# Performance work log

Measured on AMD Instinct MI355X. Metric: run time of the kernel, lower is better.

Reference implementation:

```python
import jax, jax.numpy as jnp
import numpy as np

D_CLAMP = 10.0
EPS = 1e-4
Z = 10.0


def setup_inputs() -> dict:
    key = jax.random.key(0)
    ks = jax.random.split(key, 7)
    b, N = 2, 512
    return {
        "predicted_rotations": jax.random.normal(ks[0], (b, N, 3, 3), dtype=jnp.float32),
        "predicted_translations": jax.random.normal(ks[1], (b, N, 3), dtype=jnp.float32),
        "predicted_atom_positions": jax.random.normal(ks[2], (b, N, 14, 3), dtype=jnp.float32),
        "atom_mask": jax.random.uniform(ks[3], (b, N, 14), dtype=jnp.float32),
        "true_rotations": jax.random.normal(ks[4], (b, N, 3, 3), dtype=jnp.float32),
        "true_translations": jax.random.normal(ks[5], (b, N, 3), dtype=jnp.float32),
        "true_atom_positions": jax.random.normal(ks[6], (b, N, 14, 3), dtype=jnp.float32),
    }


def reference(predicted_rotations, predicted_translations, predicted_atom_positions,
              atom_mask, true_rotations, true_translations, true_atom_positions):
    b, N = predicted_rotations.shape[:2]
    pred_pos = predicted_atom_positions.reshape(b, N * 14, 3)   # [b, A, 3]
    true_pos = true_atom_positions.reshape(b, N * 14, 3)
    mask = atom_mask.reshape(b, N * 14)                          # [b, A]

    # Inverse rigid transforms: R^-1 = R^T, t^-1 = -R^T t
    R_pred_inv = jnp.swapaxes(predicted_rotations, -1, -2)       # [b, N, 3, 3]
    t_pred_inv = -jnp.einsum('birc,bic->bir', R_pred_inv, predicted_translations)
    R_true_inv = jnp.swapaxes(true_rotations, -1, -2)
    t_true_inv = -jnp.einsum('birc,bic->bir', R_true_inv, true_translations)

    # Express every atom in every frame's local coordinates: [b, N, A, 3]
    x_frames_pred = jnp.einsum('biop,bjp->bijo', R_pred_inv, pred_pos) + t_pred_inv[:, :, None, :]
    x_frames_true = jnp.einsum('biop,bjp->bijo', R_true_inv, true_pos) + t_true_inv[:, :, None, :]

    dist = jnp.sqrt(jnp.sum((x_frames_pred - x_frames_true) ** 2, axis=-1) + EPS)  # [b, N, A]
    dist_clamped = jnp.minimum(dist, D_CLAMP)

    n_atoms = jnp.maximum(jnp.sum(mask, axis=-1, keepdims=True), 1.0)              # [b, 1]
    frame_means = jnp.sum(dist_clamped * mask[:, None, :], axis=-1) / n_atoms      # [b, N]
    fape_loss = jnp.mean(frame_means, axis=-1) / Z                                 # [b]
    return fape_loss
```

## Files before the change

kernel.cpp:

```cpp
#include <hip/hip_runtime.h>

#define FAPE_EPS   1e-4f
#define FAPE_CLAMP 10.0f
#define FAPE_Z     10.0f

constexpr int TPB   = 256;
constexpr int FPB   = 8;
constexpr int APT   = 8;
constexpr int ATILE = TPB * APT;
constexpr int GRPSZ = 16;
constexpr int MAXG  = 1024;

typedef float v2f __attribute__((ext_vector_type(2)));
static __device__ __forceinline__ v2f splat2(float x) { return (v2f){x, x}; }

__device__ unsigned g_gt[MAXG] = {};
__device__ unsigned g_st       = 0;

__device__ __forceinline__ v2f blockReduce2(v2f v, v2f* swave, int tid) {
    for (int off = 32; off > 0; off >>= 1) {
        v.x += __shfl_down(v.x, off);
        v.y += __shfl_down(v.y, off);
    }
    if ((tid & 63) == 0) swave[tid >> 6] = v;
    __syncthreads();
    v2f s = (v2f){0.f, 0.f};
    if (tid == 0) {
#pragma unroll
        for (int w = 0; w < TPB / 64; ++w) s += swave[w];
    }
    __syncthreads();
    return s;
}

__global__ __launch_bounds__(TPB) void fape_fused_kernel(
        const float* __restrict__ Rp, const float* __restrict__ tp,
        const float* __restrict__ pp, const float* __restrict__ mask,
        const float* __restrict__ Rt, const float* __restrict__ tt,
        const float* __restrict__ pt, float* __restrict__ out,
        float* __restrict__ ws, int N, int A,
        int fTilesPerBatch, int atomTiles, int b,
        unsigned nBlocks, unsigned nGroups) {

    const int tid   = threadIdx.x;
    const int t     = blockIdx.x;
    const int atile = t % atomTiles;
    const int ft    = t / atomTiles;
    const int batch = ft / fTilesPerBatch;
    const int ftile = ft % fTilesPerBatch;
    const int f0    = ftile * FPB;
    const int P     = fTilesPerBatch * atomTiles;

    float* __restrict__ partial  = ws;
    float* __restrict__ maskPart = ws + nBlocks;

    const float* __restrict__ ppb = pp   + (size_t)batch * A * 3;
    const float* __restrict__ ptb = pt   + (size_t)batch * A * 3;
    const float* __restrict__ mb  = mask + (size_t)batch * A;

    v2f pX[4], pY[4], pZ[4], qX[4], qY[4], qZ[4], m2[4];
    const int j0 = atile * ATILE + tid * APT;
    if (j0 + APT <= A) {
        const float4* p4 = reinterpret_cast<const float4*>(ppb + (size_t)j0 * 3);
        const float4* q4 = reinterpret_cast<const float4*>(ptb + (size_t)j0 * 3);
        const float4 P0 = p4[0], P1 = p4[1], P2 = p4[2];
        const float4 P3 = p4[3], P4 = p4[4], P5 = p4[5];
        const float4 Q0 = q4[0], Q1 = q4[1], Q2 = q4[2];
        const float4 Q3 = q4[3], Q4 = q4[4], Q5 = q4[5];
        const float4 M0 = *reinterpret_cast<const float4*>(mb + j0);
        const float4 M1 = *reinterpret_cast<const float4*>(mb + j0 + 4);
        pX[0]=(v2f){P0.x,P0.w}; pY[0]=(v2f){P0.y,P1.x}; pZ[0]=(v2f){P0.z,P1.y};
        pX[1]=(v2f){P1.z,P2.y}; pY[1]=(v2f){P1.w,P2.z}; pZ[1]=(v2f){P2.x,P2.w};
        pX[2]=(v2f){P3.x,P3.w}; pY[2]=(v2f){P3.y,P4.x}; pZ[2]=(v2f){P3.z,P4.y};
        pX[3]=(v2f){P4.z,P5.y}; pY[3]=(v2f){P4.w,P5.z}; pZ[3]=(v2f){P5.x,P5.w};
        qX[0]=(v2f){Q0.x,Q0.w}; qY[0]=(v2f){Q0.y,Q1.x}; qZ[0]=(v2f){Q0.z,Q1.y};
        qX[1]=(v2f){Q1.z,Q2.y}; qY[1]=(v2f){Q1.w,Q2.z}; qZ[1]=(v2f){Q2.x,Q2.w};
        qX[2]=(v2f){Q3.x,Q3.w}; qY[2]=(v2f){Q3.y,Q4.x}; qZ[2]=(v2f){Q3.z,Q4.y};
        qX[3]=(v2f){Q4.z,Q5.y}; qY[3]=(v2f){Q4.w,Q5.z}; qZ[3]=(v2f){Q5.x,Q5.w};
        m2[0]=(v2f){M0.x,M0.y}; m2[1]=(v2f){M0.z,M0.w};
        m2[2]=(v2f){M1.x,M1.y}; m2[3]=(v2f){M1.z,M1.w};
    } else {
        float ps[APT][3], qs[APT][3], ms[APT];
#pragma unroll
        for (int k = 0; k < APT; ++k) {
            const int j = j0 + k;
            if (j < A) {
                ps[k][0]=ppb[j*3+0]; ps[k][1]=ppb[j*3+1]; ps[k][2]=ppb[j*3+2];
                qs[k][0]=ptb[j*3+0]; qs[k][1]=ptb[j*3+1]; qs[k][2]=ptb[j*3+2];
                ms[k]=mb[j];
            } else {
                ps[k][0]=ps[k][1]=ps[k][2]=0.f;
                qs[k][0]=qs[k][1]=qs[k][2]=0.f;
                ms[k]=0.f;
            }
        }
#pragma unroll
        for (int g = 0; g < 4; ++g) {
            pX[g]=(v2f){ps[2*g][0], ps[2*g+1][0]};
            pY[g]=(v2f){ps[2*g][1], ps[2*g+1][1]};
            pZ[g]=(v2f){ps[2*g][2], ps[2*g+1][2]};
            qX[g]=(v2f){qs[2*g][0], qs[2*g+1][0]};
            qY[g]=(v2f){qs[2*g][1], qs[2*g+1][1]};
            qZ[g]=(v2f){qs[2*g][2], qs[2*g+1][2]};
            m2[g]=(v2f){ms[2*g], ms[2*g+1]};
        }
    }

    const v2f epsv   = splat2(FAPE_EPS);
    const v2f clampv = splat2(FAPE_CLAMP);
    v2f lacc = (v2f){0.f, 0.f};
    for (int f = 0; f < FPB; ++f) {
        const int fl = f0 + f;
        if (fl < N) {
            const size_t fi = (size_t)batch * N + fl;
            const float* __restrict__ rp = Rp + fi * 9;
            const float* __restrict__ rt = Rt + fi * 9;
            const float* __restrict__ tv = tp + fi * 3;
            const float* __restrict__ uv = tt + fi * 3;

            const float rp00=rp[0], rp01=rp[1], rp02=rp[2];
            const float rp10=rp[3], rp11=rp[4], rp12=rp[5];
            const float rp20=rp[6], rp21=rp[7], rp22=rp[8];
            const float rt00=rt[0], rt01=rt[1], rt02=rt[2];
            const float rt10=rt[3], rt11=rt[4], rt12=rt[5];
            const float rt20=rt[6], rt21=rt[7], rt22=rt[8];
            const float tp0=tv[0], tp1=tv[1], tp2=tv[2];
            const float tt0=uv[0], tt1=uv[1], tt2=uv[2];

            const float c0 = rt00*tt0 + rt10*tt1 + rt20*tt2 - (rp00*tp0 + rp10*tp1 + rp20*tp2);
            const float c1 = rt01*tt0 + rt11*tt1 + rt21*tt2 - (rp01*tp0 + rp11*tp1 + rp21*tp2);
            const float c2 = rt02*tt0 + rt12*tt1 + rt22*tt2 - (rp02*tp0 + rp12*tp1 + rp22*tp2);
            const v2f c0v = splat2(c0), c1v = splat2(c1), c2v = splat2(c2);

#pragma unroll
            for (int g = 0; g < 4; ++g) {
                v2f x0 = c0v + rp00*pX[g] + rp10*pY[g] + rp20*pZ[g]
                             - (rt00*qX[g] + rt10*qY[g] + rt20*qZ[g]);
                v2f x1 = c1v + rp01*pX[g] + rp11*pY[g] + rp21*pZ[g]
                             - (rt01*qX[g] + rt11*qY[g] + rt21*qZ[g]);
                v2f x2 = c2v + rp02*pX[g] + rp12*pY[g] + rp22*pZ[g]
                             - (rt02*qX[g] + rt12*qY[g] + rt22*qZ[g]);
                v2f d2 = epsv + x0*x0 + x1*x1 + x2*x2;
                v2f dmin = (v2f){
                    fminf(__builtin_amdgcn_sqrtf(d2.x), clampv.x),
                    fminf(__builtin_amdgcn_sqrtf(d2.y), clampv.y)};
                lacc += dmin * m2[g];
            }
        }
    }

    __shared__ v2f  swave2[TPB / 64];
    __shared__ bool sLast;

    const float msum_in = (ftile == 0)
        ? (m2[0].x + m2[0].y + m2[1].x + m2[1].y +
           m2[2].x + m2[2].y + m2[3].x + m2[3].y) : 0.f;
    const v2f red = blockReduce2((v2f){lacc.x + lacc.y, msum_in}, swave2, tid);
    const float bs = red.x, mbs = red.y;

    if (tid == 0) {
        sLast = false;

        __hip_atomic_store(&partial[t], bs,
                           __ATOMIC_RELAXED, __HIP_MEMORY_SCOPE_AGENT);
        if (ftile == 0)
            __hip_atomic_store(&maskPart[batch * atomTiles + atile], mbs,
                               __ATOMIC_RELAXED, __HIP_MEMORY_SCOPE_AGENT);

        asm volatile("s_waitcnt vmcnt(0)" ::: "memory");

        const unsigned g     = (unsigned)t / GRPSZ;
        const unsigned gbase = g * GRPSZ;
        const unsigned gsz   = (nBlocks - gbase < (unsigned)GRPSZ)
                                   ? (nBlocks - gbase) : (unsigned)GRPSZ;
        const unsigned old = __hip_atomic_fetch_add(&g_gt[g], 1u,
                                  __ATOMIC_RELAXED, __HIP_MEMORY_SCOPE_AGENT);
        if (old == gsz - 1u) {
            const unsigned old2 = __hip_atomic_fetch_add(&g_st, 1u,
                                       __ATOMIC_RELAXED, __HIP_MEMORY_SCOPE_AGENT);
            if (old2 == nGroups - 1u) sLast = true;
        }
    }
    __syncthreads();
    if (!sLast) return;

    for (int bb = 0; bb < b; ++bb) {
        const float* __restrict__ pb = partial + (size_t)bb * P;
        float v0 = 0.f, v1 = 0.f, mv = 0.f;
        if (tid < P)
            v0 = __hip_atomic_load(&pb[tid], __ATOMIC_RELAXED, __HIP_MEMORY_SCOPE_AGENT);
        if (tid + TPB < P)
            v1 = __hip_atomic_load(&pb[tid + TPB], __ATOMIC_RELAXED, __HIP_MEMORY_SCOPE_AGENT);
        if (tid < atomTiles)
            mv = __hip_atomic_load(&maskPart[bb * atomTiles + tid],
                                   __ATOMIC_RELAXED, __HIP_MEMORY_SCOPE_AGENT);

        const v2f r = blockReduce2((v2f){v0 + v1, mv}, swave2, tid);
        if (tid == 0)
            out[bb] = r.x / (fmaxf(r.y, 1.0f) * (float)N * FAPE_Z);
    }

    for (unsigned i = tid; i < nGroups; i += TPB)
        __hip_atomic_store(&g_gt[i], 0u, __ATOMIC_RELAXED, __HIP_MEMORY_SCOPE_AGENT);
    if (tid == 0)
        __hip_atomic_store(&g_st, 0u, __ATOMIC_RELAXED, __HIP_MEMORY_SCOPE_AGENT);
}

extern "C" void kernel_launch(void* const* d_in, const int* in_sizes, int n_in,
                              void* d_out, int out_size, void* d_ws, size_t ws_size,
                              hipStream_t stream) {
    const float* Rp   = (const float*)d_in[0];
    const float* tp   = (const float*)d_in[1];
    const float* pp   = (const float*)d_in[2];
    const float* mask = (const float*)d_in[3];
    const float* Rt   = (const float*)d_in[4];
    const float* tt   = (const float*)d_in[5];
    const float* pt   = (const float*)d_in[6];
    float* out = (float*)d_out;
    float* ws  = (float*)d_ws;

    const int b  = out_size;
    const int bN = in_sizes[1] / 3;
    const int N  = bN / b;
    const int A  = N * 14;

    const int fTilesPerBatch = (N + FPB - 1) / FPB;
    const int atomTiles      = (A + ATILE - 1) / ATILE;
    const unsigned nBlocks   = (unsigned)(b * fTilesPerBatch * atomTiles);
    const unsigned nGroups   = (nBlocks + GRPSZ - 1) / GRPSZ;

    fape_fused_kernel<<<dim3(nBlocks), dim3(TPB), 0, stream>>>(
        Rp, tp, pp, mask, Rt, tt, pt, out, ws,
        N, A, fTilesPerBatch, atomTiles, b, nBlocks, nGroups);
}
```

Before: 16.56 us.

## Clamp squared distance before sqrt, unroll full frame tiles, batch final reduction

Clamps the squared distance against CLAMP² before taking the square root, which is equivalent because both functions are monotonic. Adds a fully unrolled fast path for frame tiles that lie entirely in range. Uses a single-value block reduction in blocks that do not contribute to the mask sum. The last block now reduces two batches at once with a 4-wide reduction and loops over partials, so P larger than 2*TPB is handled; this adds code size and register use.

```diff
diff --git a/kernel.cpp b/kernel.cpp
--- a/kernel.cpp
+++ b/kernel.cpp
@@ -12,22 +12,54 @@
 constexpr int MAXG  = 1024;
 
 typedef float v2f __attribute__((ext_vector_type(2)));
+typedef float v4f __attribute__((ext_vector_type(4)));
 static __device__ __forceinline__ v2f splat2(float x) { return (v2f){x, x}; }
 
 __device__ unsigned g_gt[MAXG] = {};
 __device__ unsigned g_st       = 0;
 
-__device__ __forceinline__ v2f blockReduce2(v2f v, v2f* swave, int tid) {
+__device__ __forceinline__ float blockReduce1(float v, float* sw, int tid) {
+    for (int off = 32; off > 0; off >>= 1) v += __shfl_down(v, off);
+    if ((tid & 63) == 0) sw[tid >> 6] = v;
+    __syncthreads();
+    float s = 0.f;
+    if (tid == 0) {
+#pragma unroll
+        for (int w = 0; w < TPB / 64; ++w) s += sw[w];
+    }
+    __syncthreads();
+    return s;
+}
+
+__device__ __forceinline__ v2f blockReduce2(v2f v, v2f* sw, int tid) {
     for (int off = 32; off > 0; off >>= 1) {
         v.x += __shfl_down(v.x, off);
         v.y += __shfl_down(v.y, off);
     }
-    if ((tid & 63) == 0) swave[tid >> 6] = v;
+    if ((tid & 63) == 0) sw[tid >> 6] = v;
     __syncthreads();
     v2f s = (v2f){0.f, 0.f};
     if (tid == 0) {
 #pragma unroll
-        for (int w = 0; w < TPB / 64; ++w) s += swave[w];
+        for (int w = 0; w < TPB / 64; ++w) s += sw[w];
+    }
+    __syncthreads();
+    return s;
+}
+
+__device__ __forceinline__ v4f blockReduce4(v4f v, v4f* sw, int tid) {
+    for (int off = 32; off > 0; off >>= 1) {
+        v.x += __shfl_down(v.x, off);
+        v.y += __shfl_down(v.y, off);
+        v.z += __shfl_down(v.z, off);
+        v.w += __shfl_down(v.w, off);
+    }
+    if ((tid & 63) == 0) sw[tid >> 6] = v;
+    __syncthreads();
+    v4f s = (v4f){0.f, 0.f, 0.f, 0.f};
+    if (tid == 0) {
+#pragma unroll
+        for (int w = 0; w < TPB / 64; ++w) s += sw[w];
     }
     __syncthreads();
     return s;
@@ -106,57 +138,69 @@
         }
     }
 
-    const v2f epsv   = splat2(FAPE_EPS);
-    const v2f clampv = splat2(FAPE_CLAMP);
+    const v2f epsv    = splat2(FAPE_EPS);
+    const v2f clamp2v = splat2(FAPE_CLAMP * FAPE_CLAMP);
     v2f lacc = (v2f){0.f, 0.f};
-    for (int f = 0; f < FPB; ++f) {
-        const int fl = f0 + f;
-        if (fl < N) {
-            const size_t fi = (size_t)batch * N + fl;
-            const float* __restrict__ rp = Rp + fi * 9;
-            const float* __restrict__ rt = Rt + fi * 9;
-            const float* __restrict__ tv = tp + fi * 3;
-            const float* __restrict__ uv = tt + fi * 3;
-
-            const float rp00=rp[0], rp01=rp[1], rp02=rp[2];
-            const float rp10=rp[3], rp11=rp[4], rp12=rp[5];
-            const float rp20=rp[6], rp21=rp[7], rp22=rp[8];
-            const float rt00=rt[0], rt01=rt[1], rt02=rt[2];
-            const float rt10=rt[3], rt11=rt[4], rt12=rt[5];
-            const float rt20=rt[6], rt21=rt[7], rt22=rt[8];
-            const float tp0=tv[0], tp1=tv[1], tp2=tv[2];
-            const float tt0=uv[0], tt1=uv[1], tt2=uv[2];
-
-            const float c0 = rt00*tt0 + rt10*tt1 + rt20*tt2 - (rp00*tp0 + rp10*tp1 + rp20*tp2);
-            const float c1 = rt01*tt0 + rt11*tt1 + rt21*tt2 - (rp01*tp0 + rp11*tp1 + rp21*tp2);
-            const float c2 = rt02*tt0 + rt12*tt1 + rt22*tt2 - (rp02*tp0 + rp12*tp1 + rp22*tp2);
-            const v2f c0v = splat2(c0), c1v = splat2(c1), c2v = splat2(c2);
-
-#pragma unroll
-            for (int g = 0; g < 4; ++g) {
-                v2f x0 = c0v + rp00*pX[g] + rp10*pY[g] + rp20*pZ[g]
-                             - (rt00*qX[g] + rt10*qY[g] + rt20*qZ[g]);
-                v2f x1 = c1v + rp01*pX[g] + rp11*pY[g] + rp21*pZ[g]
-                             - (rt01*qX[g] + rt11*qY[g] + rt21*qZ[g]);
-                v2f x2 = c2v + rp02*pX[g] + rp12*pY[g] + rp22*pZ[g]
-                             - (rt02*qX[g] + rt12*qY[g] + rt22*qZ[g]);
-                v2f d2 = epsv + x0*x0 + x1*x1 + x2*x2;
-                v2f dmin = (v2f){
-                    fminf(__builtin_amdgcn_sqrtf(d2.x), clampv.x),
-                    fminf(__builtin_amdgcn_sqrtf(d2.y), clampv.y)};
-                lacc += dmin * m2[g];
-            }
-        }
-    }
-
-    __shared__ v2f  swave2[TPB / 64];
-    __shared__ bool sLast;
-
-    const float msum_in = (ftile == 0)
-        ? (m2[0].x + m2[0].y + m2[1].x + m2[1].y +
-           m2[2].x + m2[2].y + m2[3].x + m2[3].y) : 0.f;
-    const v2f red = blockReduce2((v2f){lacc.x + lacc.y, msum_in}, swave2, tid);
-    const float bs = red.x, mbs = red.y;
+
+    auto doFrame = [&](int fl) {
+        const size_t fi = (size_t)batch * N + fl;
+        const float* __restrict__ rp = Rp + fi * 9;
+        const float* __restrict__ rt = Rt + fi * 9;
+        const float* __restrict__ tv = tp + fi * 3;
+        const float* __restrict__ uv = tt + fi * 3;
+
+        const float rp00=rp[0], rp01=rp[1], rp02=rp[2];
+        const float rp10=rp[3], rp11=rp[4], rp12=rp[5];
+        const float rp20=rp[6], rp21=rp[7], rp22=rp[8];
+        const float rt00=rt[0], rt01=rt[1], rt02=rt[2];
+        const float rt10=rt[3], rt11=rt[4], rt12=rt[5];
+        const float rt20=rt[6], rt21=rt[7], rt22=rt[8];
+        const float tp0=tv[0], tp1=tv[1], tp2=tv[2];
+        const float tt0=uv[0], tt1=uv[1], tt2=uv[2];
+
+        const float c0 = rt00*tt0 + rt10*tt1 + rt20*tt2 - (rp00*tp0 + rp10*tp1 + rp20*tp2);
+        const float c1 = rt01*tt0 + rt11*tt1 + rt21*tt2 - (rp01*tp0 + rp11*tp1 + rp21*tp2);
+        const float c2 = rt02*tt0 + rt12*tt1 + rt22*tt2 - (rp02*tp0 + rp12*tp1 + rp22*tp2);
+        const v2f c0v = splat2(c0), c1v = splat2(c1), c2v = splat2(c2);
+
+#pragma unroll
+        for (int g = 0; g < 4; ++g) {
+            v2f x0 = c0v + rp00*pX[g] + rp10*pY[g] + rp20*pZ[g]
+                         - (rt00*qX[g] + rt10*qY[g] + rt20*qZ[g]);
+            v2f x1 = c1v + rp01*pX[g] + rp11*pY[g] + rp21*pZ[g]
+                         - (rt01*qX[g] + rt11*qY[g] + rt21*qZ[g]);
+            v2f x2 = c2v + rp02*pX[g] + rp12*pY[g] + rp22*pZ[g]
+                         - (rt02*qX[g] + rt12*qY[g] + rt22*qZ[g]);
+            v2f d2 = epsv + x0*x0 + x1*x1 + x2*x2;
+            d2 = (v2f){fminf(d2.x, clamp2v.x), fminf(d2.y, clamp2v.y)};
+            const v2f dmin = (v2f){__builtin_amdgcn_sqrtf(d2.x),
+                                   __builtin_amdgcn_sqrtf(d2.y)};
+            lacc += dmin * m2[g];
+        }
+    };
+
+    if (f0 + FPB <= N) {
+#pragma unroll
+        for (int f = 0; f < FPB; ++f) doFrame(f0 + f);
+    } else {
+        for (int f = 0; f < FPB; ++f)
+            if (f0 + f < N) doFrame(f0 + f);
+    }
+
+    __shared__ float swaveS[TPB / 64];
+    __shared__ v2f   swave2[TPB / 64];
+    __shared__ v4f   swave4[TPB / 64];
+    __shared__ bool  sLast;
+
+    float bs, mbs = 0.f;
+    if (ftile == 0) {
+        const float msum_in = m2[0].x + m2[0].y + m2[1].x + m2[1].y +
+                              m2[2].x + m2[2].y + m2[3].x + m2[3].y;
+        const v2f r = blockReduce2((v2f){lacc.x + lacc.y, msum_in}, swave2, tid);
+        bs = r.x; mbs = r.y;
+    } else {
+        bs = blockReduce1(lacc.x + lacc.y, swaveS, tid);
+    }
 
     if (tid == 0) {
         sLast = false;
@@ -184,18 +228,36 @@
     __syncthreads();
     if (!sLast) return;
 
-    for (int bb = 0; bb < b; ++bb) {
+    int bb = 0;
+    for (; bb + 2 <= b; bb += 2) {
+        const float* __restrict__ pb0 = partial + (size_t)bb * P;
+        const float* __restrict__ pb1 = partial + (size_t)(bb + 1) * P;
+        float v0 = 0.f, v1 = 0.f, mv0 = 0.f, mv1 = 0.f;
+        for (int i = tid; i < P; i += TPB) {
+            v0 += __hip_atomic_load(&pb0[i], __ATOMIC_RELAXED, __HIP_MEMORY_SCOPE_AGENT);
+            v1 += __hip_atomic_load(&pb1[i], __ATOMIC_RELAXED, __HIP_MEMORY_SCOPE_AGENT);
+        }
+        if (tid < atomTiles) {
+            mv0 = __hip_atomic_load(&maskPart[bb * atomTiles + tid],
+                                    __ATOMIC_RELAXED, __HIP_MEMORY_SCOPE_AGENT);
+            mv1 = __hip_atomic_load(&maskPart[(bb + 1) * atomTiles + tid],
+                                    __ATOMIC_RELAXED, __HIP_MEMORY_SCOPE_AGENT);
+        }
+        const v4f r = blockReduce4((v4f){v0, mv0, v1, mv1}, swave4, tid);
+        if (tid == 0) {
+            out[bb]     = r.x / (fmaxf(r.y, 1.0f) * (float)N * FAPE_Z);
+            out[bb + 1] = r.z / (fmaxf(r.w, 1.0f) * (float)N * FAPE_Z);
+        }
+    }
+    for (; bb < b; ++bb) {
         const float* __restrict__ pb = partial + (size_t)bb * P;
-        float v0 = 0.f, v1 = 0.f, mv = 0.f;
-        if (tid < P)
-            v0 = __hip_atomic_load(&pb[tid], __ATOMIC_RELAXED, __HIP_MEMORY_SCOPE_AGENT);
-        if (tid + TPB < P)
-            v1 = __hip_atomic_load(&pb[tid + TPB], __ATOMIC_RELAXED, __HIP_MEMORY_SCOPE_AGENT);
+        float v0 = 0.f, mv = 0.f;
+        for (int i = tid; i < P; i += TPB)
+            v0 += __hip_atomic_load(&pb[i], __ATOMIC_RELAXED, __HIP_MEMORY_SCOPE_AGENT);
         if (tid < atomTiles)
             mv = __hip_atomic_load(&maskPart[bb * atomTiles + tid],
                                    __ATOMIC_RELAXED, __HIP_MEMORY_SCOPE_AGENT);
-
-        const v2f r = blockReduce2((v2f){v0 + v1, mv}, swave2, tid);
+        const v2f r = blockReduce2((v2f){v0, mv}, swave2, tid);
         if (tid == 0)
             out[bb] = r.x / (fmaxf(r.y, 1.0f) * (float)N * FAPE_Z);
     }
```

Result: no change. 16.29 us (-1.6%).
